# Kernel optimization log

Measured on AMD Instinct MI355X. Metric: run time of the kernel, lower is better.

## Reference

```python
import jax, jax.numpy as jnp
import numpy as np

NC = 80
NA = 3
BOX_GAIN, CLS_GAIN, OBJ_GAIN = 7.5, 0.5, 1.0
GAMMA = 1.5
LS = 0.0
EPS = 1e-7
ANCHORS = np.array([[[10, 13], [16, 30], [33, 23]],
                    [[30, 61], [62, 45], [59, 119]],
                    [[116, 90], [156, 198], [373, 326]]], dtype=np.float32)


def bce_logits(x, t):
    # numerically stable BCE-with-logits, elementwise
    return jnp.maximum(x, 0.0) - x * t + jnp.log1p(jnp.exp(-jnp.abs(x)))


def iou_cxcywh(b1, b2, eps=EPS):
    b1x1, b1x2 = b1[..., 0] - b1[..., 2] / 2, b1[..., 0] + b1[..., 2] / 2
    b1y1, b1y2 = b1[..., 1] - b1[..., 3] / 2, b1[..., 1] + b1[..., 3] / 2
    b2x1, b2x2 = b2[..., 0] - b2[..., 2] / 2, b2[..., 0] + b2[..., 2] / 2
    b2y1, b2y2 = b2[..., 1] - b2[..., 3] / 2, b2[..., 1] + b2[..., 3] / 2
    inter = jnp.clip(jnp.minimum(b1x2, b2x2) - jnp.maximum(b1x1, b2x1), 0.0) * \
            jnp.clip(jnp.minimum(b1y2, b2y2) - jnp.maximum(b1y1, b2y1), 0.0)
    w1, h1 = b1x2 - b1x1, b1y2 - b1y1 + eps
    w2, h2 = b2x2 - b2x1, b2y2 - b2y1 + eps
    union = w1 * h1 + w2 * h2 - inter + eps
    return inter / union


def _scale_loss(pred, targets, anchors):
    B, C, h, w = pred.shape
    p = pred.reshape(B, NA, NC + 5, h, w).transpose(0, 1, 3, 4, 2)  # [B,3,h,w,nc+5]
    pobj = p[..., 4]

    N = targets.shape[0]
    scale = jnp.array([w, h, w, h], dtype=pred.dtype)
    g = targets[:, 2:6] * scale  # grid-space cx,cy,w,h
    gx, gy = g[:, 0], g[:, 1]
    valid = (gx >= 0) & (gx < w) & (gy >= 0) & (gy < h)
    gi = jnp.clip(jnp.floor(gx).astype(jnp.int32), 0, w - 1)
    gj = jnp.clip(jnp.floor(gy).astype(jnp.int32), 0, h - 1)
    bidx = jnp.clip(targets[:, 0].astype(jnp.int32), 0, B - 1)
    cls = jnp.clip(targets[:, 1].astype(jnp.int32), 0, NC - 1)

    # each GT is assigned to all 3 anchors -> M = 3N rows
    rep = lambda v: jnp.repeat(v, NA, axis=0)
    bM, giM, gjM, clsM, maskM = rep(bidx), rep(gi), rep(gj), rep(cls), rep(valid)
    aiM = jnp.tile(jnp.arange(NA), N)
    anchM = anchors[aiM]                             # [M,2]
    txyM = rep(g[:, :2] - jnp.floor(g[:, :2]))       # cell-relative offsets
    twhM = rep(g[:, 2:4])
    mf = maskM.astype(pred.dtype)
    n_valid = mf.sum()

    # objectness target grid (duplicates collapse to 1 via max, like repeated set)
    tobj = jnp.zeros((B, NA, h, w), pred.dtype).at[bM, aiM, gjM, giM].max(mf)
    loss_obj = bce_logits(pobj, tobj).mean() * OBJ_GAIN

    ps = p[bM, aiM, gjM, giM]                        # [M, nc+5]
    ps_box, ps_cls = ps[:, :4], ps[:, 5:]

    # focal classification loss
    t = jax.nn.one_hot(clsM, NC, dtype=pred.dtype)
    if LS > 0:
        t = t * (1 - LS) + LS / NC
    ce = bce_logits(ps_cls, t)
    focal = (1.0 - jnp.exp(-ce)) ** GAMMA * ce       # [M, nc]
    row_sum = (focal * mf[:, None]).sum(-1)          # [M]
    loss_cls = jnp.where(n_valid > 0,
                         row_sum.sum() / (jnp.maximum(n_valid, 1.0) * NC),
                         0.0) * CLS_GAIN

    # per-class focal means (rows grouped by GT class)
    seg_ids = jnp.where(maskM, clsM, NC)
    seg_sum = jax.ops.segment_sum(row_sum, seg_ids, num_segments=NC + 1)[:NC]
    seg_cnt = jax.ops.segment_sum(mf, seg_ids, num_segments=NC + 1)[:NC]
    per_class = jnp.where(seg_cnt > 0,
                          seg_sum / (jnp.maximum(seg_cnt, 1.0) * NC),
                          0.0) * CLS_GAIN

    # box (IoU) loss
    pxy = jax.nn.sigmoid(ps_box[:, :2]) * 2.0 - 0.5
    pwh = (jax.nn.sigmoid(ps_box[:, 2:4]) * 2.0) ** 2 * anchM
    pbox = jnp.concatenate([pxy, pwh], axis=-1)
    tbox = jnp.concatenate([txyM, twhM], axis=-1)
    iou = iou_cxcywh(pbox, tbox)
    loss_box = jnp.where(n_valid > 0,
                         ((1.0 - iou) * mf).sum() / jnp.maximum(n_valid, 1.0),
                         0.0) * BOX_GAIN

    return loss_box, loss_cls, loss_obj, per_class


def setup_inputs() -> dict:
    key = jax.random.key(0)
    k0, k1, k2, kb, kc, kxy, kwh = jax.random.split(key, 7)
    B, N = 16, 800
    p0 = jax.random.normal(k0, (B, NA * (NC + 5), 80, 80), jnp.float32)
    p1 = jax.random.normal(k1, (B, NA * (NC + 5), 40, 40), jnp.float32)
    p2 = jax.random.normal(k2, (B, NA * (NC + 5), 20, 20), jnp.float32)
    bcol = jax.random.randint(kb, (N, 1), 0, B).astype(jnp.float32)
    ccol = jax.random.randint(kc, (N, 1), 0, NC).astype(jnp.float32)
    xy = jax.random.uniform(kxy, (N, 2), jnp.float32, 0.02, 0.98)
    wh = jax.random.uniform(kwh, (N, 2), jnp.float32, 0.02, 0.30)
    targets = jnp.concatenate([bcol, ccol, xy, wh], axis=1)  # [N,6]
    return {"p0": p0, "p1": p1, "p2": p2, "targets": targets}


def reference(p0, p1, p2, targets):
    anchors = jnp.asarray(ANCHORS)
    lb = lc = lo = 0.0
    pc = jnp.zeros((NC,), jnp.float32)
    for i, pred in enumerate((p0, p1, p2)):
        b, c, o, per_class = _scale_loss(pred, targets, anchors[i])
        lb, lc, lo = lb + b, lc + c, lo + o
        pc = pc + per_class
    total = lb + lc + lo
    # [loss, loss_box, loss_cls, loss_obj, per-class cls losses...]
    return jnp.concatenate([jnp.stack([total, lb, lc, lo]), pc])
```

## Files before the change

### kernel.cpp

```cpp
#include <hip/hip_runtime.h>
#include <math.h>

#define NC 80
#define TCOLS 6
#define OBJ_BLOCKS 61
#define HSIZE 4096

__device__ __constant__ float c_anch[3][3][2] = {
  {{10.f,13.f},{16.f,30.f},{33.f,23.f}},
  {{30.f,61.f},{62.f,45.f},{59.f,119.f}},
  {{116.f,90.f},{156.f,198.f},{373.f,326.f}}
};

#define ACC_CORR   0
#define ACC_BOX(s) (16 + 16*(s))
#define ACC_CLS(s) (64 + 16*(s))
#define ACC_NV(s)  (112 + 16*(s))
#define ACC_SEG    160
#define ACC_TOTAL  (160 + 6*NC)

__device__ __forceinline__ float fbce0(float x) {
  return fmaxf(x, 0.f) + __logf(1.f + __expf(-fabsf(x)));
}
__device__ __forceinline__ float fbce(float x, float t) {
  return fmaxf(x, 0.f) - x * t + __logf(1.f + __expf(-fabsf(x)));
}
__device__ __forceinline__ float ffocal(float x, float t) {
  float ce = fbce(x, t);
  float u  = 1.f - __expf(-ce);
  return u * __builtin_amdgcn_sqrtf(u) * ce;
}

__global__ void k_init(float* __restrict__ acc) {
  for (int k = threadIdx.x; k < ACC_TOTAL; k += 256) acc[k] = 0.f;
}

__global__ __launch_bounds__(1024, 8)
void k_fused(const float* __restrict__ p0, const float* __restrict__ p1,
             const float* __restrict__ p2, const float* __restrict__ tgt,
             int N, int B, int RB, float* __restrict__ acc,
             float* __restrict__ partial) {
  const int bid = blockIdx.x;
  const int tid = threadIdx.x;

  if (bid < RB) {
    __shared__ float l_box[3], l_cls[3], l_nv[3];
    if (tid < 3) { l_box[tid]=0.f; l_cls[tid]=0.f; l_nv[tid]=0.f; }
    __syncthreads();
    int row   = bid * 16 + (tid >> 6);
    int lane  = tid & 63;
    int nrows = 9 * N;
    if (row < nrows) {
      int rps = N * 3;
      int s   = row / rps;
      int rem = row - s * rps;
      int n   = rem / 3;
      int a   = rem - n * 3;
      int w   = (s == 0) ? 80 : ((s == 1) ? 40 : 20);
      int hw  = w * w;
      const float* pred = (s == 0) ? p0 : ((s == 1) ? p1 : p2);
      float fw = (float)w;
      float gx = tgt[n*TCOLS + 2] * fw, gy = tgt[n*TCOLS + 3] * fw;
      if (gx >= 0.f && gx < fw && gy >= 0.f && gy < fw) {
        float gw = tgt[n*TCOLS + 4] * fw, gh = tgt[n*TCOLS + 5] * fw;
        int gi  = min(max((int)floorf(gx), 0), w - 1);
        int gj  = min(max((int)floorf(gy), 0), w - 1);
        int b   = min(max((int)tgt[n*TCOLS + 0], 0), B - 1);
        int cls = min(max((int)tgt[n*TCOLS + 1], 0), NC - 1);
        size_t base = (size_t)(b*255 + a*85) * hw + (size_t)(gj*w + gi);

        float x0  = pred[base + (size_t)(5 + lane) * hw];
        float x1  = (lane < 16) ? pred[base + (size_t)(69 + lane) * hw] : 0.f;
        float bxv = (lane < 4)  ? pred[base + (size_t)lane * hw] : 0.f;

        float rs = ffocal(x0, (lane == cls) ? 1.f : 0.f);
        if (lane < 16) rs += ffocal(x1, ((64 + lane) == cls) ? 1.f : 0.f);
        for (int off = 32; off > 0; off >>= 1) rs += __shfl_xor(rs, off, 64);

        float bx = __shfl(bxv, 0, 64), by = __shfl(bxv, 1, 64);
        float bw = __shfl(bxv, 2, 64), bh = __shfl(bxv, 3, 64);
        if (lane == 0) {
          float sx = 1.f/(1.f + __expf(-bx));
          float sy = 1.f/(1.f + __expf(-by));
          float sw = 1.f/(1.f + __expf(-bw));
          float sh = 1.f/(1.f + __expf(-bh));
          float px = sx*2.f - 0.5f, py = sy*2.f - 0.5f;
          float aw = c_anch[s][a][0], ah = c_anch[s][a][1];
          float pw = (sw*2.f)*(sw*2.f)*aw, ph = (sh*2.f)*(sh*2.f)*ah;
          float txf = gx - floorf(gx), tyf = gy - floorf(gy);
          float b1x1 = px - pw*0.5f, b1x2 = px + pw*0.5f;
          float b1y1 = py - ph*0.5f, b1y2 = py + ph*0.5f;
          float b2x1 = txf - gw*0.5f, b2x2 = txf + gw*0.5f;
          float b2y1 = tyf - gh*0.5f, b2y2 = tyf + gh*0.5f;
          float iw = fmaxf(fminf(b1x2, b2x2) - fmaxf(b1x1, b2x1), 0.f);
          float ih = fmaxf(fminf(b1y2, b2y2) - fmaxf(b1y1, b2y1), 0.f);
          float inter = iw * ih;
          float w1 = b1x2 - b1x1, h1 = b1y2 - b1y1 + 1e-7f;
          float w2 = b2x2 - b2x1, h2 = b2y2 - b2y1 + 1e-7f;
          float uni = w1*h1 + w2*h2 - inter + 1e-7f;
          float iou = inter / uni;

          atomicAdd(&l_box[s], 1.f - iou);
          atomicAdd(&l_cls[s], rs);
          atomicAdd(&l_nv[s],  1.f);
          atomicAdd(&acc[ACC_SEG +        s*NC + cls], rs);
          atomicAdd(&acc[ACC_SEG + 3*NC + s*NC + cls], 1.f);
        }
      }
    }
    __syncthreads();
    if (tid < 3) {
      int s = tid; float v;
      v = l_box[s]; if (v != 0.f) atomicAdd(&acc[ACC_BOX(s)], v);
      v = l_cls[s]; if (v != 0.f) atomicAdd(&acc[ACC_CLS(s)], v);
      v = l_nv [s]; if (v != 0.f) atomicAdd(&acc[ACC_NV (s)], v);
    }
  } else if (bid < RB + OBJ_BLOCKS) {
    const int ob = bid - RB;
    const int n0 = B*3*6400, n1 = B*3*1600, n2 = B*3*400;
    const int total4 = (n0 + n1 + n2) >> 2;
    const float i0 = 1.f/(float)n0, i1 = 1.f/(float)n1, i2 = 1.f/(float)n2;
    float local = 0.f;
    for (int i = ob * 1024 + tid; i < total4; i += OBJ_BLOCKS * 1024) {
      int e = i << 2;
      const float* pred; int idx, hw; float inv;
      if (e < n0)         { pred = p0; idx = e;           hw = 6400; inv = i0; }
      else if (e < n0+n1) { pred = p1; idx = e - n0;      hw = 1600; inv = i1; }
      else                { pred = p2; idx = e - n0 - n1; hw = 400;  inv = i2; }
      int ba = idx / hw, pix = idx - ba * hw;
      int b = ba / 3, a = ba - b * 3;
      const float4 x4 = *(const float4*)&pred[(size_t)(b*255 + a*85 + 4) * hw + pix];
      local += (fbce0(x4.x) + fbce0(x4.y) + fbce0(x4.z) + fbce0(x4.w)) * inv;
    }
    for (int off = 32; off > 0; off >>= 1) local += __shfl_xor(local, off, 64);
    __shared__ float red[16];
    if ((tid & 63) == 0) red[tid >> 6] = local;
    __syncthreads();
    if (tid == 0) {
      float t = 0.f;
      for (int k = 0; k < 16; ++k) t += red[k];
      partial[ob] = t;
    }
  } else {
    __shared__ int htab[HSIZE];
    __shared__ float cred[16];
    for (int k = tid; k < HSIZE; k += 1024) htab[k] = -1;
    __syncthreads();
    int M = 3 * N;
    float corr = 0.f;
    for (int i = tid; i < M; i += 1024) {
      int s = i / N, n = i - s * N;
      int w = (s == 0) ? 80 : ((s == 1) ? 40 : 20);
      float fw = (float)w;
      float gx = tgt[n*TCOLS + 2] * fw, gy = tgt[n*TCOLS + 3] * fw;
      if (gx >= 0.f && gx < fw && gy >= 0.f && gy < fw) {
        int hw = w * w;
        int gi = min(max((int)floorf(gx), 0), w - 1);
        int gj = min(max((int)floorf(gy), 0), w - 1);
        int b  = min(max((int)tgt[n*TCOLS + 0], 0), B - 1);
        int idx = b * hw + gj * w + gi;
        int key = (s << 17) | idx;
        unsigned h = ((unsigned)key * 2654435761u) >> 20;
        bool owner = false;
        for (;;) {
          int old = atomicCAS(&htab[h & (HSIZE-1)], -1, key);
          if (old == -1)  { owner = true; break; }
          if (old == key) { break; }
          ++h;
        }
        if (owner) {
          const float* pred = (s == 0) ? p0 : ((s == 1) ? p1 : p2);
          int cell = idx - b * hw;
          float inv = 1.f / (float)(B * 3 * hw);
          float sum = pred[(size_t)(b*255 +   4) * hw + cell]
                    + pred[(size_t)(b*255 +  89) * hw + cell]
                    + pred[(size_t)(b*255 + 174) * hw + cell];
          corr -= sum * inv;
        }
      }
    }
    for (int off = 32; off > 0; off >>= 1) corr += __shfl_xor(corr, off, 64);
    if ((tid & 63) == 0) cred[tid >> 6] = corr;
    __syncthreads();
    if (tid == 0) {
      float t = 0.f;
      for (int k = 0; k < 16; ++k) t += cred[k];
      acc[ACC_CORR] = t;
    }
  }
}

__global__ void k_final(const float* __restrict__ acc, const float* __restrict__ partial,
                        float* __restrict__ out) {
  __shared__ float slo;
  int t = threadIdx.x;
  float v = (t < OBJ_BLOCKS) ? partial[t] : 0.f;
  for (int off = 32; off > 0; off >>= 1) v += __shfl_xor(v, off, 64);
  if (t == 0) slo = v;
  __syncthreads();
  if (t == 0) {
    float lo = slo + acc[ACC_CORR];
    float lb = 0.f, lc = 0.f;
    for (int s = 0; s < 3; ++s) {
      float nv  = acc[ACC_NV(s)];
      float nvm = fmaxf(nv, 1.f);
      if (nv > 0.f) {
        lb += acc[ACC_BOX(s)] / nvm * 7.5f;
        lc += acc[ACC_CLS(s)] / (nvm * (float)NC) * 0.5f;
      }
    }
    out[0] = lb + lc + lo;
    out[1] = lb;
    out[2] = lc;
    out[3] = lo;
  }
  if (t < NC) {
    float pc = 0.f;
    for (int s = 0; s < 3; ++s) {
      float cnt = acc[ACC_SEG + 3*NC + s*NC + t];
      if (cnt > 0.f)
        pc += acc[ACC_SEG + s*NC + t] / (fmaxf(cnt, 1.f) * (float)NC) * 0.5f;
    }
    out[4 + t] = pc;
  }
}

extern "C" void kernel_launch(void* const* d_in, const int* in_sizes, int n_in,
                              void* d_out, int out_size, void* d_ws, size_t ws_size,
                              hipStream_t stream) {
  const float* p0  = (const float*)d_in[0];
  const float* p1  = (const float*)d_in[1];
  const float* p2  = (const float*)d_in[2];
  const float* tgt = (const float*)d_in[3];
  int N = in_sizes[3] / TCOLS;
  int B = in_sizes[0] / (255 * 6400);
  float* out = (float*)d_out;

  float* acc     = (float*)d_ws;
  float* partial = acc + ACC_TOTAL;

  int nrows = 9 * N;
  int RB = (nrows + 15) / 16;
  int grid = RB + OBJ_BLOCKS + 1;

  k_init <<<1, 256, 0, stream>>>(acc);
  k_fused<<<grid, 1024, 0, stream>>>(p0, p1, p2, tgt, N, B, RB, acc, partial);
  k_final<<<1, 128, 0, stream>>>(acc, partial, out);
}
```

Before: 41.87 us.

## Parallelize objectness correction with a global bitmask instead of a single-block hash

The objectness correction, which undoes the zero-target term at assigned cells, used to run in one block that deduplicated cells through a shared-memory CAS hash table. It now runs across 40 blocks, one thread per (target, scale, anchor) row, and deduplicates with atomicOr on a global bitmask over every (batch, anchor, cell). The bitmask is cleared by a wider k_init. The obj-streaming block count also drops from 61 to 22, and the corr and obj blocks are placed ahead of the row blocks in the grid. The aim is to remove the serial single-block tail, at the cost of an extra ~50KB memset and global atomics.

```diff
diff --git a/kernel.cpp b/kernel.cpp
--- a/kernel.cpp
+++ b/kernel.cpp
@@ -3,8 +3,8 @@
 
 #define NC 80
 #define TCOLS 6
-#define OBJ_BLOCKS 61
-#define HSIZE 4096
+#define CORRB 40
+#define OBJB  22
 
 __device__ __constant__ float c_anch[3][3][2] = {
   {{10.f,13.f},{16.f,30.f},{33.f,23.f}},
@@ -31,23 +31,28 @@
   return u * __builtin_amdgcn_sqrtf(u) * ce;
 }
 
-__global__ void k_init(float* __restrict__ acc) {
-  for (int k = threadIdx.x; k < ACC_TOTAL; k += 256) acc[k] = 0.f;
+__global__ void k_init(unsigned int* __restrict__ mask, int nwords,
+                       float* __restrict__ acc) {
+  int i  = blockIdx.x * blockDim.x + threadIdx.x;
+  int st = gridDim.x * blockDim.x;
+  for (int k = i; k < nwords;    k += st) mask[k] = 0u;
+  for (int k = i; k < ACC_TOTAL; k += st) acc[k]  = 0.f;
 }
 
 __global__ __launch_bounds__(1024, 8)
 void k_fused(const float* __restrict__ p0, const float* __restrict__ p1,
              const float* __restrict__ p2, const float* __restrict__ tgt,
-             int N, int B, int RB, float* __restrict__ acc,
-             float* __restrict__ partial) {
+             unsigned int* __restrict__ mask, int N, int B,
+             float* __restrict__ acc, float* __restrict__ partial) {
   const int bid = blockIdx.x;
   const int tid = threadIdx.x;
-
-  if (bid < RB) {
-    __shared__ float l_box[3], l_cls[3], l_nv[3];
+  __shared__ float red[16];
+  __shared__ float l_box[3], l_cls[3], l_nv[3];
+
+  if (bid >= CORRB + OBJB) {
     if (tid < 3) { l_box[tid]=0.f; l_cls[tid]=0.f; l_nv[tid]=0.f; }
     __syncthreads();
-    int row   = bid * 16 + (tid >> 6);
+    int row   = (bid - CORRB - OBJB) * 16 + (tid >> 6);
     int lane  = tid & 63;
     int nrows = 9 * N;
     if (row < nrows) {
@@ -115,13 +120,13 @@
       v = l_cls[s]; if (v != 0.f) atomicAdd(&acc[ACC_CLS(s)], v);
       v = l_nv [s]; if (v != 0.f) atomicAdd(&acc[ACC_NV (s)], v);
     }
-  } else if (bid < RB + OBJ_BLOCKS) {
-    const int ob = bid - RB;
+  } else if (bid >= CORRB) {
+    const int ob = bid - CORRB;
     const int n0 = B*3*6400, n1 = B*3*1600, n2 = B*3*400;
     const int total4 = (n0 + n1 + n2) >> 2;
     const float i0 = 1.f/(float)n0, i1 = 1.f/(float)n1, i2 = 1.f/(float)n2;
     float local = 0.f;
-    for (int i = ob * 1024 + tid; i < total4; i += OBJ_BLOCKS * 1024) {
+    for (int i = ob * 1024 + tid; i < total4; i += OBJB * 1024) {
       int e = i << 2;
       const float* pred; int idx, hw; float inv;
       if (e < n0)         { pred = p0; idx = e;           hw = 6400; inv = i0; }
@@ -133,7 +138,6 @@
       local += (fbce0(x4.x) + fbce0(x4.y) + fbce0(x4.z) + fbce0(x4.w)) * inv;
     }
     for (int off = 32; off > 0; off >>= 1) local += __shfl_xor(local, off, 64);
-    __shared__ float red[16];
     if ((tid & 63) == 0) red[tid >> 6] = local;
     __syncthreads();
     if (tid == 0) {
@@ -142,14 +146,12 @@
       partial[ob] = t;
     }
   } else {
-    __shared__ int htab[HSIZE];
-    __shared__ float cred[16];
-    for (int k = tid; k < HSIZE; k += 1024) htab[k] = -1;
-    __syncthreads();
-    int M = 3 * N;
+    int i = bid * 1024 + tid;
     float corr = 0.f;
-    for (int i = tid; i < M; i += 1024) {
-      int s = i / N, n = i - s * N;
+    int M = 9 * N;
+    if (i < M) {
+      int n = i / 9, r = i - n * 9;
+      int s = r / 3, a = r - s * 3;
       int w = (s == 0) ? 80 : ((s == 1) ? 40 : 20);
       float fw = (float)w;
       float gx = tgt[n*TCOLS + 2] * fw, gy = tgt[n*TCOLS + 3] * fw;
@@ -158,34 +160,24 @@
         int gi = min(max((int)floorf(gx), 0), w - 1);
         int gj = min(max((int)floorf(gy), 0), w - 1);
         int b  = min(max((int)tgt[n*TCOLS + 0], 0), B - 1);
-        int idx = b * hw + gj * w + gi;
-        int key = (s << 17) | idx;
-        unsigned h = ((unsigned)key * 2654435761u) >> 20;
-        bool owner = false;
-        for (;;) {
-          int old = atomicCAS(&htab[h & (HSIZE-1)], -1, key);
-          if (old == -1)  { owner = true; break; }
-          if (old == key) { break; }
-          ++h;
-        }
-        if (owner) {
+        int basebit = (s == 0) ? 0 : ((s == 1) ? B*3*6400 : B*3*8000);
+        int bit = basebit + (b*3 + a)*hw + gj*w + gi;
+        unsigned int m = 1u << (bit & 31);
+        unsigned int old = atomicOr(&mask[bit >> 5], m);
+        if (!(old & m)) {
           const float* pred = (s == 0) ? p0 : ((s == 1) ? p1 : p2);
-          int cell = idx - b * hw;
-          float inv = 1.f / (float)(B * 3 * hw);
-          float sum = pred[(size_t)(b*255 +   4) * hw + cell]
-                    + pred[(size_t)(b*255 +  89) * hw + cell]
-                    + pred[(size_t)(b*255 + 174) * hw + cell];
-          corr -= sum * inv;
+          float x = pred[(size_t)(b*255 + a*85 + 4) * hw + (size_t)(gj*w + gi)];
+          corr -= x / (float)(B * 3 * hw);
         }
       }
     }
     for (int off = 32; off > 0; off >>= 1) corr += __shfl_xor(corr, off, 64);
-    if ((tid & 63) == 0) cred[tid >> 6] = corr;
+    if ((tid & 63) == 0) red[tid >> 6] = corr;
     __syncthreads();
     if (tid == 0) {
       float t = 0.f;
-      for (int k = 0; k < 16; ++k) t += cred[k];
-      acc[ACC_CORR] = t;
+      for (int k = 0; k < 16; ++k) t += red[k];
+      if (t != 0.f) atomicAdd(&acc[ACC_CORR], t);
     }
   }
 }
@@ -194,7 +186,7 @@
                         float* __restrict__ out) {
   __shared__ float slo;
   int t = threadIdx.x;
-  float v = (t < OBJ_BLOCKS) ? partial[t] : 0.f;
+  float v = (t < OBJB) ? partial[t] : 0.f;
   for (int off = 32; off > 0; off >>= 1) v += __shfl_xor(v, off, 64);
   if (t == 0) slo = v;
   __syncthreads();
@@ -236,14 +228,17 @@
   int B = in_sizes[0] / (255 * 6400);
   float* out = (float*)d_out;
 
-  float* acc     = (float*)d_ws;
+  unsigned int* mask = (unsigned int*)d_ws;
+  int nbits  = B * 3 * (6400 + 1600 + 400);
+  int nwords = (nbits + 31) / 32;
+  float* acc     = (float*)((char*)d_ws + (((size_t)nwords * 4 + 255) & ~(size_t)255));
   float* partial = acc + ACC_TOTAL;
 
   int nrows = 9 * N;
   int RB = (nrows + 15) / 16;
-  int grid = RB + OBJ_BLOCKS + 1;
-
-  k_init <<<1, 256, 0, stream>>>(acc);
-  k_fused<<<grid, 1024, 0, stream>>>(p0, p1, p2, tgt, N, B, RB, acc, partial);
+  int grid = CORRB + OBJB + RB;
+
+  k_init <<<64, 256, 0, stream>>>(mask, nwords, acc);
+  k_fused<<<grid, 1024, 0, stream>>>(p0, p1, p2, tgt, mask, N, B, acc, partial);
   k_final<<<1, 128, 0, stream>>>(acc, partial, out);
 }
```

After: 37.19 us. 11.2% less time.
